# Optimization experiments

Hardware: AMD Instinct MI355X
Metric: run time of the kernel (lower is better)

Reference implementation:

```python
import jax, jax.numpy as jnp
import numpy as np

INPUT_SIZE = 2048
HIDDEN_SIZE = 2048
BATCH = 4096
COMBINED = INPUT_SIZE + HIDDEN_SIZE


def setup_inputs() -> dict:
    key = jax.random.key(0)
    ks = jax.random.split(key, 11)
    s = 1.0 / np.sqrt(COMBINED)  # torch Linear default init scale
    inp = {
        "x_t": jax.random.normal(ks[0], (BATCH, INPUT_SIZE), jnp.float32),
        "h_prev": jax.random.normal(ks[1], (BATCH, HIDDEN_SIZE), jnp.float32),
        "c_prev": jax.random.normal(ks[2], (BATCH, HIDDEN_SIZE), jnp.float32),
        # torch nn.Linear weights: [out, in]
        "W_f": jax.random.uniform(ks[3], (HIDDEN_SIZE, COMBINED), jnp.float32, -s, s),
        "b_f": jax.random.uniform(ks[4], (HIDDEN_SIZE,), jnp.float32, -s, s),
        "W_i": jax.random.uniform(ks[5], (HIDDEN_SIZE, COMBINED), jnp.float32, -s, s),
        "b_i": jax.random.uniform(ks[6], (HIDDEN_SIZE,), jnp.float32, -s, s),
        "W_c": jax.random.uniform(ks[7], (HIDDEN_SIZE, COMBINED), jnp.float32, -s, s),
        "b_c": jax.random.uniform(ks[8], (HIDDEN_SIZE,), jnp.float32, -s, s),
        "W_o": jax.random.uniform(ks[9], (HIDDEN_SIZE, COMBINED), jnp.float32, -s, s),
        "b_o": jax.random.uniform(ks[10], (HIDDEN_SIZE,), jnp.float32, -s, s),
    }
    return inp


def reference(x_t, h_prev, c_prev, W_f, b_f, W_i, b_i, W_c, b_c, W_o, b_o):
    # combined = cat([h_prev, x_t], dim=1)  -> [B, H + I]
    combined = jnp.concatenate([h_prev, x_t], axis=1)
    # Fuse the four gate GEMMs into one [B, C] x [C, 4H] matmul.
    W = jnp.concatenate([W_f, W_i, W_c, W_o], axis=0)  # [4H, C]
    b = jnp.concatenate([b_f, b_i, b_c, b_o], axis=0)  # [4H]
    gates = combined @ W.T + b  # [B, 4H]
    gf, gi, gc, go = jnp.split(gates, 4, axis=1)
    f_t = jax.nn.sigmoid(gf)
    i_t = jax.nn.sigmoid(gi)
    c_tilde = jnp.tanh(gc)
    o_t = jax.nn.sigmoid(go)
    c_t = f_t * c_prev + i_t * c_tilde
    h_t = o_t * jnp.tanh(c_t)
    return (h_t, c_t)
```

## Files before the change

### kernel.cpp

```cpp
#include <hip/hip_runtime.h>
#include <hip/hip_bf16.h>
#include <cstdint>

#define B_DIM 4096
#define H_DIM 2048
#define I_DIM 2048
#define K_DIM 4096
#define N4    8192

typedef unsigned int u32;
typedef unsigned short u16;
typedef __attribute__((ext_vector_type(4))) float floatx4;
typedef __attribute__((ext_vector_type(8))) short bf16x8;
typedef __attribute__((ext_vector_type(8))) float f32x8;
typedef __attribute__((ext_vector_type(8))) __bf16 bfx8;

__device__ static inline void gload16(const void* g, void* l) {
    __builtin_amdgcn_global_load_lds(
        (const __attribute__((address_space(1))) u32*)g,
        (__attribute__((address_space(3))) u32*)l, 16, 0, 0);
}
__device__ static inline float fast_sig(float x) {
    return 1.f / (1.f + __expf(-x));
}
__device__ static inline float fast_tanh(float x) {
    float ax = fabsf(x);
    float t = __expf(-2.f * ax);
    float r = (1.f - t) / (1.f + t);
    return copysignf(r, x);
}

__global__ void convert_all(const float* __restrict__ h_prev, const float* __restrict__ x_t,
                            const float* __restrict__ Wf, const float* __restrict__ Wi,
                            const float* __restrict__ Wc, const float* __restrict__ Wo,
                            u16* __restrict__ comb, u16* __restrict__ wb) {
    const int bid = blockIdx.x;
    const float* src;
    u16* dst;
    if (bid < 8192) {
        int base = (bid * 256 + (int)threadIdx.x) * 8;
        int row = base >> 12, col = base & 4095;
        src = (col < H_DIM) ? h_prev + (size_t)row * H_DIM + col
                            : x_t    + (size_t)row * I_DIM + (col - H_DIM);
        dst = comb + base;
    } else {
        long long base = ((long long)(bid - 8192) * 256 + threadIdx.x) * 8;
        int n = (int)(base >> 12), col = (int)(base & 4095);
        int row128 = n & 127;
        int g = (row128 >> 4) & 3;
        int j = (n >> 7) * 32 + ((row128 >> 6) << 4) + (row128 & 15);
        const float* W = (g == 0) ? Wf : (g == 1) ? Wi : (g == 2) ? Wc : Wo;
        src = W + (size_t)j * K_DIM + col;
        dst = wb + base;
    }
    float4 v0 = *(const float4*)src;
    float4 v1 = *(const float4*)(src + 4);
    f32x8 f = { v0.x, v0.y, v0.z, v0.w, v1.x, v1.y, v1.z, v1.w };
    *(bfx8*)dst = __builtin_convertvector(f, bfx8);
}

__device__ static inline void stage32(const u16* __restrict__ A, const u16* __restrict__ Bm,
                                      u16* dA, u16* dB, int mb, int nbT, int kt, int tid) {
#pragma unroll
    for (int s = 0; s < 2; ++s) {
        int c = tid + s * 512;
        int row = c >> 2;
        int ko = ((c & 3) ^ ((c >> 3) & 3)) * 8;
        gload16(A + (size_t)(mb + row) * K_DIM + kt + ko, (char*)dA + c * 16);
        gload16(Bm + (size_t)(nbT + row) * K_DIM + kt + ko, (char*)dB + c * 16);
    }
}

__global__ __launch_bounds__(512, 2) void gemm_lstm(const u16* __restrict__ A,
                                                    const u16* __restrict__ Bm,
                                                    const float* __restrict__ c_prev,
                                                    const float* __restrict__ bf_,
                                                    const float* __restrict__ bi_,
                                                    const float* __restrict__ bc_,
                                                    const float* __restrict__ bo_,
                                                    float* __restrict__ out) {
    __shared__ __align__(16) u16 lsA[4][256 * 32];
    __shared__ __align__(16) u16 lsB[4][256 * 32];

    const int tid  = threadIdx.x;
    const int lane = tid & 63;
    const int wave = tid >> 6;
    const int wm2  = (wave >> 2) * 128;
    const int wn2  = (wave & 3) * 64;
    const int quad = lane >> 4;
    const int r    = lane & 15;
    const int qsw  = (quad ^ ((r >> 1) & 3)) * 8;
    const int mb   = blockIdx.y * 256;
    const int nbT  = blockIdx.x * 256;

    floatx4 acc[8][4];
#pragma unroll
    for (int i = 0; i < 8; ++i)
#pragma unroll
        for (int g = 0; g < 4; ++g)
            acc[i][g] = (floatx4){0.f, 0.f, 0.f, 0.f};

#pragma unroll
    for (int pt = 0; pt < 3; ++pt)
        stage32(A, Bm, lsA[pt], lsB[pt], mb, nbT, pt * 32, tid);

#pragma unroll 4
    for (int t = 0; t < 128; ++t) {
        if (t < 126) {
            asm volatile("s_waitcnt vmcnt(8)" ::: "memory");
        } else {
            asm volatile("s_waitcnt vmcnt(0)" ::: "memory");
        }
        __builtin_amdgcn_s_barrier();
        __builtin_amdgcn_sched_barrier(0);

        if (t < 125)
            stage32(A, Bm, lsA[(t + 3) & 3], lsB[(t + 3) & 3], mb, nbT, (t + 3) * 32, tid);

        const u16* sA = lsA[t & 3];
        const u16* sB = lsB[t & 3];
        bf16x8 af[8], bb[4];
#pragma unroll
        for (int i = 0; i < 8; ++i)
            af[i] = *(const bf16x8*)&sA[(wm2 + i * 16 + r) * 32 + qsw];
#pragma unroll
        for (int g = 0; g < 4; ++g)
            bb[g] = *(const bf16x8*)&sB[(wn2 + g * 16 + r) * 32 + qsw];

        __builtin_amdgcn_s_setprio(1);
#pragma unroll
        for (int i = 0; i < 8; ++i)
#pragma unroll
            for (int g = 0; g < 4; ++g)
                acc[i][g] = __builtin_amdgcn_mfma_f32_16x16x32_bf16(
                    af[i], bb[g], acc[i][g], 0, 0, 0);
        __builtin_amdgcn_s_setprio(0);
    }

    __builtin_amdgcn_sched_barrier(0);

    const int j = blockIdx.x * 64 + (wave & 3) * 16 + r;
    const float bfv = bf_[j], biv = bi_[j], bcv = bc_[j], bov = bo_[j];
    const int rowb = mb + wm2 + quad * 4;
    const float* cp = c_prev + (size_t)rowb * H_DIM + j;
    float* oh = out + (size_t)rowb * H_DIM + j;
    float* oc = oh + (size_t)B_DIM * H_DIM;
#pragma unroll
    for (int i = 0; i < 8; ++i) {
#pragma unroll
        for (int rg = 0; rg < 4; ++rg) {
            size_t off = (size_t)(i * 16 + rg) * H_DIM;
            float gf = acc[i][0][rg] + bfv;
            float gi = acc[i][1][rg] + biv;
            float gc = acc[i][2][rg] + bcv;
            float go = acc[i][3][rg] + bov;
            float f  = fast_sig(gf);
            float ii = fast_sig(gi);
            float ct = fast_tanh(gc);
            float oo = fast_sig(go);
            float c  = f * cp[off] + ii * ct;
            float h  = oo * fast_tanh(c);
            oh[off] = h;
            oc[off] = c;
        }
    }
}

__global__ void lstm_naive(const float* __restrict__ x_t, const float* __restrict__ h_prev,
                           const float* __restrict__ c_prev,
                           const float* __restrict__ Wf, const float* __restrict__ bf_,
                           const float* __restrict__ Wi, const float* __restrict__ bi_,
                           const float* __restrict__ Wc, const float* __restrict__ bc_,
                           const float* __restrict__ Wo, const float* __restrict__ bo_,
                           float* __restrict__ out) {
    int j = blockIdx.x * blockDim.x + threadIdx.x;
    int b = blockIdx.y;
    const float* hrow = h_prev + (long long)b * H_DIM;
    const float* xrow = x_t   + (long long)b * I_DIM;
    const float* wf = Wf + (long long)j * K_DIM;
    const float* wi = Wi + (long long)j * K_DIM;
    const float* wc = Wc + (long long)j * K_DIM;
    const float* wo = Wo + (long long)j * K_DIM;
    float af = bf_[j], ai = bi_[j], ac = bc_[j], ao = bo_[j];
    for (int k = 0; k < H_DIM; k += 4) {
        float4 v = *(const float4*)(hrow + k);
        float4 a = *(const float4*)(wf + k);
        float4 bqi = *(const float4*)(wi + k);
        float4 cq = *(const float4*)(wc + k);
        float4 dq = *(const float4*)(wo + k);
        af += v.x*a.x + v.y*a.y + v.z*a.z + v.w*a.w;
        ai += v.x*bqi.x + v.y*bqi.y + v.z*bqi.z + v.w*bqi.w;
        ac += v.x*cq.x + v.y*cq.y + v.z*cq.z + v.w*cq.w;
        ao += v.x*dq.x + v.y*dq.y + v.z*dq.z + v.w*dq.w;
    }
    for (int k = 0; k < I_DIM; k += 4) {
        float4 v = *(const float4*)(xrow + k);
        float4 a = *(const float4*)(wf + H_DIM + k);
        float4 bqi = *(const float4*)(wi + H_DIM + k);
        float4 cq = *(const float4*)(wc + H_DIM + k);
        float4 dq = *(const float4*)(wo + H_DIM + k);
        af += v.x*a.x + v.y*a.y + v.z*a.z + v.w*a.w;
        ai += v.x*bqi.x + v.y*bqi.y + v.z*bqi.z + v.w*bqi.w;
        ac += v.x*cq.x + v.y*cq.y + v.z*cq.z + v.w*cq.w;
        ao += v.x*dq.x + v.y*dq.y + v.z*dq.z + v.w*dq.w;
    }
    float f  = 1.f / (1.f + __expf(-af));
    float ii = 1.f / (1.f + __expf(-ai));
    float ct = tanhf(ac);
    float oo = 1.f / (1.f + __expf(-ao));
    int t = b * H_DIM + j;
    float c = f * c_prev[t] + ii * ct;
    out[t] = oo * tanhf(c);
    out[B_DIM * H_DIM + t] = c;
}

extern "C" void kernel_launch(void* const* d_in, const int* in_sizes, int n_in,
                              void* d_out, int out_size, void* d_ws, size_t ws_size,
                              hipStream_t stream) {
    const float* x_t    = (const float*)d_in[0];
    const float* h_prev = (const float*)d_in[1];
    const float* c_prev = (const float*)d_in[2];
    const float* Wf = (const float*)d_in[3];  const float* bf_ = (const float*)d_in[4];
    const float* Wi = (const float*)d_in[5];  const float* bi_ = (const float*)d_in[6];
    const float* Wc = (const float*)d_in[7];  const float* bc_ = (const float*)d_in[8];
    const float* Wo = (const float*)d_in[9];  const float* bo_ = (const float*)d_in[10];
    float* out = (float*)d_out;

    const size_t comb_elems = (size_t)B_DIM * K_DIM;
    const size_t wb_elems   = (size_t)N4 * K_DIM;
    const size_t need = (comb_elems + wb_elems) * sizeof(u16);

    if (ws_size >= need) {
        u16* comb = (u16*)d_ws;
        u16* wb   = comb + comb_elems;
        convert_all<<<24576, 256, 0, stream>>>(h_prev, x_t, Wf, Wi, Wc, Wo, comb, wb);
        dim3 grid(N4 / 256, B_DIM / 256);
        gemm_lstm<<<grid, 512, 0, stream>>>(comb, wb, c_prev, bf_, bi_, bc_, bo_, out);
    } else {
        dim3 grid(H_DIM / 256, B_DIM);
        lstm_naive<<<grid, 256, 0, stream>>>(x_t, h_prev, c_prev,
                                             Wf, bf_, Wi, bi_, Wc, bc_, Wo, bo_, out);
    }
}
```

Before: 489.8 us.

## Double-buffer LDS fragments in GEMM main loop and grid-stride the convert kernel

The GEMM main loop now loads the next K-step's A/B fragments from LDS into a second register set while MFMAs run on the current set, a software-pipelined ping-pong with a peeled prologue and epilogue. Global-load addresses are precomputed per thread, so each stage only adds an offset. The convert kernel becomes a grid-stride loop launched with far fewer blocks. The aim is to hide LDS read latency behind MFMA and cut address and launch overhead, at the cost of more VGPRs, which may hurt occupancy at 2 blocks of 512 threads.

```diff
diff --git a/kernel.cpp b/kernel.cpp
--- a/kernel.cpp
+++ b/kernel.cpp
@@ -30,46 +30,69 @@
     return copysignf(r, x);
 }
 
-__global__ void convert_all(const float* __restrict__ h_prev, const float* __restrict__ x_t,
-                            const float* __restrict__ Wf, const float* __restrict__ Wi,
-                            const float* __restrict__ Wc, const float* __restrict__ Wo,
-                            u16* __restrict__ comb, u16* __restrict__ wb) {
-    const int bid = blockIdx.x;
-    const float* src;
-    u16* dst;
-    if (bid < 8192) {
-        int base = (bid * 256 + (int)threadIdx.x) * 8;
-        int row = base >> 12, col = base & 4095;
-        src = (col < H_DIM) ? h_prev + (size_t)row * H_DIM + col
-                            : x_t    + (size_t)row * I_DIM + (col - H_DIM);
-        dst = comb + base;
-    } else {
-        long long base = ((long long)(bid - 8192) * 256 + threadIdx.x) * 8;
-        int n = (int)(base >> 12), col = (int)(base & 4095);
-        int row128 = n & 127;
-        int g = (row128 >> 4) & 3;
-        int j = (n >> 7) * 32 + ((row128 >> 6) << 4) + (row128 & 15);
-        const float* W = (g == 0) ? Wf : (g == 1) ? Wi : (g == 2) ? Wc : Wo;
-        src = W + (size_t)j * K_DIM + col;
-        dst = wb + base;
-    }
-    float4 v0 = *(const float4*)src;
-    float4 v1 = *(const float4*)(src + 4);
-    f32x8 f = { v0.x, v0.y, v0.z, v0.w, v1.x, v1.y, v1.z, v1.w };
-    *(bfx8*)dst = __builtin_convertvector(f, bfx8);
-}
-
-__device__ static inline void stage32(const u16* __restrict__ A, const u16* __restrict__ Bm,
-                                      u16* dA, u16* dB, int mb, int nbT, int kt, int tid) {
-#pragma unroll
-    for (int s = 0; s < 2; ++s) {
-        int c = tid + s * 512;
-        int row = c >> 2;
-        int ko = ((c & 3) ^ ((c >> 3) & 3)) * 8;
-        gload16(A + (size_t)(mb + row) * K_DIM + kt + ko, (char*)dA + c * 16);
-        gload16(Bm + (size_t)(nbT + row) * K_DIM + kt + ko, (char*)dB + c * 16);
-    }
-}
+__global__ __launch_bounds__(256) void convert_all(
+        const float* __restrict__ h_prev, const float* __restrict__ x_t,
+        const float* __restrict__ Wf, const float* __restrict__ Wi,
+        const float* __restrict__ Wc, const float* __restrict__ Wo,
+        u16* __restrict__ comb, u16* __restrict__ wb) {
+    const long long NCHUNK = ((long long)B_DIM * K_DIM + (long long)N4 * K_DIM) / 8;
+    for (long long ci = (long long)blockIdx.x * 256 + threadIdx.x; ci < NCHUNK;
+         ci += (long long)gridDim.x * 256) {
+        long long e = ci * 8;
+        const float* src;
+        u16* dst;
+        if (e < (long long)B_DIM * K_DIM) {
+            int base = (int)e;
+            int row = base >> 12, col = base & 4095;
+            src = (col < H_DIM) ? h_prev + (size_t)row * H_DIM + col
+                                : x_t    + (size_t)row * I_DIM + (col - H_DIM);
+            dst = comb + base;
+        } else {
+            long long base = e - (long long)B_DIM * K_DIM;
+            int n = (int)(base >> 12), col = (int)(base & 4095);
+            int row128 = n & 127;
+            int g = (row128 >> 4) & 3;
+            int j = (n >> 7) * 32 + ((row128 >> 6) << 4) + (row128 & 15);
+            const float* W = (g == 0) ? Wf : (g == 1) ? Wi : (g == 2) ? Wc : Wo;
+            src = W + (size_t)j * K_DIM + col;
+            dst = wb + base;
+        }
+        float4 v0 = *(const float4*)src;
+        float4 v1 = *(const float4*)(src + 4);
+        f32x8 f = { v0.x, v0.y, v0.z, v0.w, v1.x, v1.y, v1.z, v1.w };
+        *(bfx8*)dst = __builtin_convertvector(f, bfx8);
+    }
+}
+
+__device__ static inline void stage32(const u16* aSrc, const u16* bSrc,
+                                      char* dA, char* dB, int doff) {
+    gload16(aSrc,                dA + doff);
+    gload16(aSrc + 128 * K_DIM,  dA + doff + 8192);
+    gload16(bSrc,                dB + doff);
+    gload16(bSrc + 128 * K_DIM,  dB + doff + 8192);
+}
+
+#define GBODY(T, FCA, FCB, FNA, FNB, VMN, DOSTAGE)                               \
+  {                                                                              \
+    asm volatile("s_waitcnt vmcnt(" #VMN ")" ::: "memory");                      \
+    __builtin_amdgcn_s_barrier();                                                \
+    __builtin_amdgcn_sched_barrier(0);                                           \
+    if (DOSTAGE)                                                                 \
+      stage32(aSrc + ((T) + 3) * 32, bSrc + ((T) + 3) * 32,                      \
+              (char*)lsA[((T) + 3) & 3], (char*)lsB[((T) + 3) & 3], doff);       \
+    const u16* sA_ = lsA[((T) + 1) & 3];                                         \
+    const u16* sB_ = lsB[((T) + 1) & 3];                                         \
+    _Pragma("unroll") for (int i_ = 0; i_ < 8; ++i_)                             \
+      FNA[i_] = *(const bf16x8*)&sA_[(wm2 + i_ * 16 + r) * 32 + qsw];            \
+    _Pragma("unroll") for (int g_ = 0; g_ < 4; ++g_)                             \
+      FNB[g_] = *(const bf16x8*)&sB_[(wn2 + g_ * 16 + r) * 32 + qsw];            \
+    __builtin_amdgcn_s_setprio(1);                                               \
+    _Pragma("unroll") for (int i_ = 0; i_ < 8; ++i_)                             \
+      _Pragma("unroll") for (int g_ = 0; g_ < 4; ++g_)                           \
+        acc[i_][g_] = __builtin_amdgcn_mfma_f32_16x16x32_bf16(                   \
+            FCA[i_], FCB[g_], acc[i_][g_], 0, 0, 0);                             \
+    __builtin_amdgcn_s_setprio(0);                                               \
+  }
 
 __global__ __launch_bounds__(512, 2) void gemm_lstm(const u16* __restrict__ A,
                                                     const u16* __restrict__ Bm,
@@ -93,6 +116,11 @@
     const int mb   = blockIdx.y * 256;
     const int nbT  = blockIdx.x * 256;
 
+    const int ko = ((tid & 3) ^ ((tid >> 3) & 3)) * 8;
+    const u16* aSrc = A  + (size_t)(mb  + (tid >> 2)) * K_DIM + ko;
+    const u16* bSrc = Bm + (size_t)(nbT + (tid >> 2)) * K_DIM + ko;
+    const int doff = tid * 16;
+
     floatx4 acc[8][4];
 #pragma unroll
     for (int i = 0; i < 8; ++i)
@@ -102,40 +130,39 @@
 
 #pragma unroll
     for (int pt = 0; pt < 3; ++pt)
-        stage32(A, Bm, lsA[pt], lsB[pt], mb, nbT, pt * 32, tid);
-
-#pragma unroll 4
-    for (int t = 0; t < 128; ++t) {
-        if (t < 126) {
-            asm volatile("s_waitcnt vmcnt(8)" ::: "memory");
-        } else {
-            asm volatile("s_waitcnt vmcnt(0)" ::: "memory");
-        }
-        __builtin_amdgcn_s_barrier();
-        __builtin_amdgcn_sched_barrier(0);
-
-        if (t < 125)
-            stage32(A, Bm, lsA[(t + 3) & 3], lsB[(t + 3) & 3], mb, nbT, (t + 3) * 32, tid);
-
-        const u16* sA = lsA[t & 3];
-        const u16* sB = lsB[t & 3];
-        bf16x8 af[8], bb[4];
+        stage32(aSrc + pt * 32, bSrc + pt * 32, (char*)lsA[pt], (char*)lsB[pt], doff);
+
+    asm volatile("s_waitcnt vmcnt(8)" ::: "memory");
+    __builtin_amdgcn_s_barrier();
+
+    bf16x8 fA0[8], fB0[4], fA1[8], fB1[4];
+    {
+        const u16* sA = lsA[0];
+        const u16* sB = lsB[0];
 #pragma unroll
         for (int i = 0; i < 8; ++i)
-            af[i] = *(const bf16x8*)&sA[(wm2 + i * 16 + r) * 32 + qsw];
+            fA0[i] = *(const bf16x8*)&sA[(wm2 + i * 16 + r) * 32 + qsw];
 #pragma unroll
         for (int g = 0; g < 4; ++g)
-            bb[g] = *(const bf16x8*)&sB[(wn2 + g * 16 + r) * 32 + qsw];
-
-        __builtin_amdgcn_s_setprio(1);
-#pragma unroll
-        for (int i = 0; i < 8; ++i)
-#pragma unroll
-            for (int g = 0; g < 4; ++g)
-                acc[i][g] = __builtin_amdgcn_mfma_f32_16x16x32_bf16(
-                    af[i], bb[g], acc[i][g], 0, 0, 0);
-        __builtin_amdgcn_s_setprio(0);
-    }
+            fB0[g] = *(const bf16x8*)&sB[(wn2 + g * 16 + r) * 32 + qsw];
+    }
+
+#pragma unroll 1
+    for (int t = 0; t < 124; t += 2) {
+        GBODY(t,     fA0, fB0, fA1, fB1, 4, 1);
+        GBODY(t + 1, fA1, fB1, fA0, fB0, 4, 1);
+    }
+    GBODY(124, fA0, fB0, fA1, fB1, 4, 1);
+    GBODY(125, fA1, fB1, fA0, fB0, 4, 0);
+    GBODY(126, fA0, fB0, fA1, fB1, 0, 0);
+    __builtin_amdgcn_s_setprio(1);
+#pragma unroll
+    for (int i = 0; i < 8; ++i)
+#pragma unroll
+        for (int g = 0; g < 4; ++g)
+            acc[i][g] = __builtin_amdgcn_mfma_f32_16x16x32_bf16(
+                fA1[i], fB1[g], acc[i][g], 0, 0, 0);
+    __builtin_amdgcn_s_setprio(0);
 
     __builtin_amdgcn_sched_barrier(0);
 
@@ -233,7 +260,7 @@
     if (ws_size >= need) {
         u16* comb = (u16*)d_ws;
         u16* wb   = comb + comb_elems;
-        convert_all<<<24576, 256, 0, stream>>>(h_prev, x_t, Wf, Wi, Wc, Wo, comb, wb);
+        convert_all<<<2048, 256, 0, stream>>>(h_prev, x_t, Wf, Wi, Wc, Wo, comb, wb);
         dim3 grid(N4 / 256, B_DIM / 256);
         gemm_lstm<<<grid, 512, 0, stream>>>(comb, wb, c_prev, bf_, bi_, bc_, bo_, out);
     } else {
```

Result: slower. 541.1 us (+10.5%).

## Fuse fp32-to-bf16 conversion into GEMM loads and drop the conversion pass

Applied to the files above, without the earlier changes.

The separate pass that converted activations and weights to bf16 in workspace is removed. The GEMM now streams fp32 tiles directly from h_prev/x_t and the four weight matrices into LDS, and converts to bf16 when building MFMA fragments. It also adds a block-index swizzle for cache locality and switches from a 4-stage to a 2-stage LDS pipeline. This saves the extra global round trip of the conversion kernel. In exchange it doubles the bytes per tile from global memory and LDS (128KB of LDS per block, which limits occupancy) and gives shallower prefetch with a full vmcnt(0) wait each step.

```diff
diff --git a/kernel.cpp b/kernel.cpp
--- a/kernel.cpp
+++ b/kernel.cpp
@@ -29,58 +29,56 @@
     float r = (1.f - t) / (1.f + t);
     return copysignf(r, x);
 }
-
-__global__ void convert_all(const float* __restrict__ h_prev, const float* __restrict__ x_t,
-                            const float* __restrict__ Wf, const float* __restrict__ Wi,
-                            const float* __restrict__ Wc, const float* __restrict__ Wo,
-                            u16* __restrict__ comb, u16* __restrict__ wb) {
-    const int bid = blockIdx.x;
-    const float* src;
-    u16* dst;
-    if (bid < 8192) {
-        int base = (bid * 256 + (int)threadIdx.x) * 8;
-        int row = base >> 12, col = base & 4095;
-        src = (col < H_DIM) ? h_prev + (size_t)row * H_DIM + col
-                            : x_t    + (size_t)row * I_DIM + (col - H_DIM);
-        dst = comb + base;
-    } else {
-        long long base = ((long long)(bid - 8192) * 256 + threadIdx.x) * 8;
-        int n = (int)(base >> 12), col = (int)(base & 4095);
-        int row128 = n & 127;
-        int g = (row128 >> 4) & 3;
-        int j = (n >> 7) * 32 + ((row128 >> 6) << 4) + (row128 & 15);
-        const float* W = (g == 0) ? Wf : (g == 1) ? Wi : (g == 2) ? Wc : Wo;
-        src = W + (size_t)j * K_DIM + col;
-        dst = wb + base;
-    }
-    float4 v0 = *(const float4*)src;
-    float4 v1 = *(const float4*)(src + 4);
-    f32x8 f = { v0.x, v0.y, v0.z, v0.w, v1.x, v1.y, v1.z, v1.w };
-    *(bfx8*)dst = __builtin_convertvector(f, bfx8);
+__device__ static inline bf16x8 pack8(float4 lo, float4 hi) {
+    f32x8 t = { lo.x, lo.y, lo.z, lo.w, hi.x, hi.y, hi.z, hi.w };
+    bfx8 b = __builtin_convertvector(t, bfx8);
+    bf16x8 rr;
+    __builtin_memcpy(&rr, &b, sizeof(rr));
+    return rr;
 }
 
-__device__ static inline void stage32(const u16* __restrict__ A, const u16* __restrict__ Bm,
-                                      u16* dA, u16* dB, int mb, int nbT, int kt, int tid) {
-#pragma unroll
-    for (int s = 0; s < 2; ++s) {
-        int c = tid + s * 512;
-        int row = c >> 2;
-        int ko = ((c & 3) ^ ((c >> 3) & 3)) * 8;
-        gload16(A + (size_t)(mb + row) * K_DIM + kt + ko, (char*)dA + c * 16);
-        gload16(Bm + (size_t)(nbT + row) * K_DIM + kt + ko, (char*)dB + c * 16);
-    }
-}
+#define STAGE(T, NA, NB)                                                        \
+  { _Pragma("unroll") for (int s_ = 0; s_ < 4; ++s_) {                          \
+      const float* sa_ = (((T) < 64) ? h_prev : xmh) + aoff[s_] + (T) * 32;     \
+      gload16(sa_, (char*)(NA) + (tid + s_ * 512) * 16);                        \
+      gload16(bptr[s_] + (T) * 32, (char*)(NB) + (tid + s_ * 512) * 16);        \
+  } }
 
-__global__ __launch_bounds__(512, 2) void gemm_lstm(const u16* __restrict__ A,
-                                                    const u16* __restrict__ Bm,
-                                                    const float* __restrict__ c_prev,
-                                                    const float* __restrict__ bf_,
-                                                    const float* __restrict__ bi_,
-                                                    const float* __restrict__ bc_,
-                                                    const float* __restrict__ bo_,
-                                                    float* __restrict__ out) {
-    __shared__ __align__(16) u16 lsA[4][256 * 32];
-    __shared__ __align__(16) u16 lsB[4][256 * 32];
+#define BODY(T, CA, CB, NA, NB)                                                 \
+  {                                                                             \
+    asm volatile("s_waitcnt vmcnt(0)" ::: "memory");                            \
+    __builtin_amdgcn_s_barrier();                                               \
+    __builtin_amdgcn_sched_barrier(0);                                          \
+    if ((T) + 1 < 128) STAGE((T) + 1, NA, NB);                                  \
+    bf16x8 af_[8], bb_[4];                                                      \
+    _Pragma("unroll") for (int i_ = 0; i_ < 8; ++i_) {                          \
+      const float* pa_ = (CA) + (wm2 + i_ * 16 + r) * 32;                       \
+      af_[i_] = pack8(*(const float4*)(pa_ + s0q), *(const float4*)(pa_ + s1q)); \
+    }                                                                           \
+    _Pragma("unroll") for (int g_ = 0; g_ < 4; ++g_) {                          \
+      const float* pb_ = (CB) + (wn2 + g_ * 16 + r) * 32;                       \
+      bb_[g_] = pack8(*(const float4*)(pb_ + s0q), *(const float4*)(pb_ + s1q)); \
+    }                                                                           \
+    __builtin_amdgcn_s_setprio(1);                                              \
+    _Pragma("unroll") for (int i_ = 0; i_ < 8; ++i_)                            \
+      _Pragma("unroll") for (int g_ = 0; g_ < 4; ++g_)                          \
+        acc[i_][g_] = __builtin_amdgcn_mfma_f32_16x16x32_bf16(                  \
+            af_[i_], bb_[g_], acc[i_][g_], 0, 0, 0);                            \
+    __builtin_amdgcn_s_setprio(0);                                              \
+  }
+
+__global__ __launch_bounds__(512, 2) void gemm_lstm(
+        const float* __restrict__ x_t, const float* __restrict__ h_prev,
+        const float* __restrict__ c_prev,
+        const float* __restrict__ Wf, const float* __restrict__ Wi,
+        const float* __restrict__ Wc, const float* __restrict__ Wo,
+        const float* __restrict__ bf_, const float* __restrict__ bi_,
+        const float* __restrict__ bc_, const float* __restrict__ bo_,
+        float* __restrict__ out) {
+    __shared__ __align__(16) float lsA0[256 * 32];
+    __shared__ __align__(16) float lsB0[256 * 32];
+    __shared__ __align__(16) float lsA1[256 * 32];
+    __shared__ __align__(16) float lsB1[256 * 32];
 
     const int tid  = threadIdx.x;
     const int lane = tid & 63;
@@ -89,9 +87,33 @@
     const int wn2  = (wave & 3) * 64;
     const int quad = lane >> 4;
     const int r    = lane & 15;
-    const int qsw  = (quad ^ ((r >> 1) & 3)) * 8;
-    const int mb   = blockIdx.y * 256;
-    const int nbT  = blockIdx.x * 256;
+    const int rx   = r & 7;
+    const int s0q  = ((2 * quad)     ^ rx) * 4;
+    const int s1q  = ((2 * quad + 1) ^ rx) * 4;
+
+    const int lin = blockIdx.y * gridDim.x + blockIdx.x;
+    const int swz = (lin & 7) * 64 + (lin >> 3);
+    const int bx  = swz & 31;
+    const int by  = swz >> 5;
+    const int mb  = by * 256;
+    const int nbT = bx * 256;
+
+    int aoff[4];
+    const float* bptr[4];
+#pragma unroll
+    for (int s = 0; s < 4; ++s) {
+        int c   = tid + s * 512;
+        int row = c >> 3;
+        int sw  = ((c & 7) ^ (row & 7)) * 4;
+        aoff[s] = (mb + row) * H_DIM + sw;
+        int n      = nbT + row;
+        int row128 = n & 127;
+        int g      = (row128 >> 4) & 3;
+        int j      = (n >> 7) * 32 + ((row128 >> 6) << 4) + (row128 & 15);
+        const float* W = (g == 0) ? Wf : (g == 1) ? Wi : (g == 2) ? Wc : Wo;
+        bptr[s] = W + (size_t)j * K_DIM + sw;
+    }
+    const float* xmh = x_t - H_DIM;
 
     floatx4 acc[8][4];
 #pragma unroll
@@ -100,46 +122,17 @@
         for (int g = 0; g < 4; ++g)
             acc[i][g] = (floatx4){0.f, 0.f, 0.f, 0.f};
 
-#pragma unroll
-    for (int pt = 0; pt < 3; ++pt)
-        stage32(A, Bm, lsA[pt], lsB[pt], mb, nbT, pt * 32, tid);
+    STAGE(0, lsA0, lsB0);
 
-#pragma unroll 4
-    for (int t = 0; t < 128; ++t) {
-        if (t < 126) {
-            asm volatile("s_waitcnt vmcnt(8)" ::: "memory");
-        } else {
-            asm volatile("s_waitcnt vmcnt(0)" ::: "memory");
-        }
-        __builtin_amdgcn_s_barrier();
-        __builtin_amdgcn_sched_barrier(0);
-
-        if (t < 125)
-            stage32(A, Bm, lsA[(t + 3) & 3], lsB[(t + 3) & 3], mb, nbT, (t + 3) * 32, tid);
-
-        const u16* sA = lsA[t & 3];
-        const u16* sB = lsB[t & 3];
-        bf16x8 af[8], bb[4];
-#pragma unroll
-        for (int i = 0; i < 8; ++i)
-            af[i] = *(const bf16x8*)&sA[(wm2 + i * 16 + r) * 32 + qsw];
-#pragma unroll
-        for (int g = 0; g < 4; ++g)
-            bb[g] = *(const bf16x8*)&sB[(wn2 + g * 16 + r) * 32 + qsw];
-
-        __builtin_amdgcn_s_setprio(1);
-#pragma unroll
-        for (int i = 0; i < 8; ++i)
-#pragma unroll
-            for (int g = 0; g < 4; ++g)
-                acc[i][g] = __builtin_amdgcn_mfma_f32_16x16x32_bf16(
-                    af[i], bb[g], acc[i][g], 0, 0, 0);
-        __builtin_amdgcn_s_setprio(0);
+#pragma unroll 1
+    for (int t = 0; t < 128; t += 2) {
+        BODY(t,     lsA0, lsB0, lsA1, lsB1);
+        BODY(t + 1, lsA1, lsB1, lsA0, lsB0);
     }
 
     __builtin_amdgcn_sched_barrier(0);
 
-    const int j = blockIdx.x * 64 + (wave & 3) * 16 + r;
+    const int j = bx * 64 + (wave & 3) * 16 + r;
     const float bfv = bf_[j], biv = bi_[j], bcv = bc_[j], bov = bo_[j];
     const int rowb = mb + wm2 + quad * 4;
     const float* cp = c_prev + (size_t)rowb * H_DIM + j;
@@ -166,54 +159,6 @@
     }
 }
 
-__global__ void lstm_naive(const float* __restrict__ x_t, const float* __restrict__ h_prev,
-                           const float* __restrict__ c_prev,
-                           const float* __restrict__ Wf, const float* __restrict__ bf_,
-                           const float* __restrict__ Wi, const float* __restrict__ bi_,
-                           const float* __restrict__ Wc, const float* __restrict__ bc_,
-                           const float* __restrict__ Wo, const float* __restrict__ bo_,
-                           float* __restrict__ out) {
-    int j = blockIdx.x * blockDim.x + threadIdx.x;
-    int b = blockIdx.y;
-    const float* hrow = h_prev + (long long)b * H_DIM;
-    const float* xrow = x_t   + (long long)b * I_DIM;
-    const float* wf = Wf + (long long)j * K_DIM;
-    const float* wi = Wi + (long long)j * K_DIM;
-    const float* wc = Wc + (long long)j * K_DIM;
-    const float* wo = Wo + (long long)j * K_DIM;
-    float af = bf_[j], ai = bi_[j], ac = bc_[j], ao = bo_[j];
-    for (int k = 0; k < H_DIM; k += 4) {
-        float4 v = *(const float4*)(hrow + k);
-        float4 a = *(const float4*)(wf + k);
-        float4 bqi = *(const float4*)(wi + k);
-        float4 cq = *(const float4*)(wc + k);
-        float4 dq = *(const float4*)(wo + k);
-        af += v.x*a.x + v.y*a.y + v.z*a.z + v.w*a.w;
-        ai += v.x*bqi.x + v.y*bqi.y + v.z*bqi.z + v.w*bqi.w;
-        ac += v.x*cq.x + v.y*cq.y + v.z*cq.z + v.w*cq.w;
-        ao += v.x*dq.x + v.y*dq.y + v.z*dq.z + v.w*dq.w;
-    }
-    for (int k = 0; k < I_DIM; k += 4) {
-        float4 v = *(const float4*)(xrow + k);
-        float4 a = *(const float4*)(wf + H_DIM + k);
-        float4 bqi = *(const float4*)(wi + H_DIM + k);
-        float4 cq = *(const float4*)(wc + H_DIM + k);
-        float4 dq = *(const float4*)(wo + H_DIM + k);
-        af += v.x*a.x + v.y*a.y + v.z*a.z + v.w*a.w;
-        ai += v.x*bqi.x + v.y*bqi.y + v.z*bqi.z + v.w*bqi.w;
-        ac += v.x*cq.x + v.y*cq.y + v.z*cq.z + v.w*cq.w;
-        ao += v.x*dq.x + v.y*dq.y + v.z*dq.z + v.w*dq.w;
-    }
-    float f  = 1.f / (1.f + __expf(-af));
-    float ii = 1.f / (1.f + __expf(-ai));
-    float ct = tanhf(ac);
-    float oo = 1.f / (1.f + __expf(-ao));
-    int t = b * H_DIM + j;
-    float c = f * c_prev[t] + ii * ct;
-    out[t] = oo * tanhf(c);
-    out[B_DIM * H_DIM + t] = c;
-}
-
 extern "C" void kernel_launch(void* const* d_in, const int* in_sizes, int n_in,
                               void* d_out, int out_size, void* d_ws, size_t ws_size,
                               hipStream_t stream) {
@@ -226,19 +171,8 @@
     const float* Wo = (const float*)d_in[9];  const float* bo_ = (const float*)d_in[10];
     float* out = (float*)d_out;
 
-    const size_t comb_elems = (size_t)B_DIM * K_DIM;
-    const size_t wb_elems   = (size_t)N4 * K_DIM;
-    const size_t need = (comb_elems + wb_elems) * sizeof(u16);
-
-    if (ws_size >= need) {
-        u16* comb = (u16*)d_ws;
-        u16* wb   = comb + comb_elems;
-        convert_all<<<24576, 256, 0, stream>>>(h_prev, x_t, Wf, Wi, Wc, Wo, comb, wb);
-        dim3 grid(N4 / 256, B_DIM / 256);
-        gemm_lstm<<<grid, 512, 0, stream>>>(comb, wb, c_prev, bf_, bi_, bc_, bo_, out);
-    } else {
-        dim3 grid(H_DIM / 256, B_DIM);
-        lstm_naive<<<grid, 256, 0, stream>>>(x_t, h_prev, c_prev,
-                                             Wf, bf_, Wi, bi_, Wc, bc_, Wo, bo_, out);
-    }
+    dim3 grid(N4 / 256, B_DIM / 256);
+    gemm_lstm<<<grid, 512, 0, stream>>>(x_t, h_prev, c_prev,
+                                        Wf, Wi, Wc, Wo,
+                                        bf_, bi_, bc_, bo_, out);
 }
```

New measurement: 713.3 us. +45.6%, slower.

## Split each K-tile into two MFMA halves interleaved with staggered global-to-LDS loads

Applied to the files above, without the earlier changes.

The 32-wide K-step body is rewritten as a macro that issues the A-tile global-to-LDS loads first and runs MFMAs on the upper 4 row-fragments. It then loads the lower A fragments, issues the B-tile loads, passes a second barrier and runs the remaining 16 MFMAs. Per-thread source and LDS addresses are precomputed once, and the final iterations are peeled so the staging branch is removed from the loop. The aim is to spread memory issue across MFMA work and reduce peak fragment register use. In exchange it adds a second workgroup barrier per tile and drops loop unrolling, which may add sync overhead.

```diff
diff --git a/kernel.cpp b/kernel.cpp
--- a/kernel.cpp
+++ b/kernel.cpp
@@ -59,17 +59,47 @@
     *(bfx8*)dst = __builtin_convertvector(f, bfx8);
 }
 
-__device__ static inline void stage32(const u16* __restrict__ A, const u16* __restrict__ Bm,
-                                      u16* dA, u16* dB, int mb, int nbT, int kt, int tid) {
-#pragma unroll
-    for (int s = 0; s < 2; ++s) {
-        int c = tid + s * 512;
-        int row = c >> 2;
-        int ko = ((c & 3) ^ ((c >> 3) & 3)) * 8;
-        gload16(A + (size_t)(mb + row) * K_DIM + kt + ko, (char*)dA + c * 16);
-        gload16(Bm + (size_t)(nbT + row) * K_DIM + kt + ko, (char*)dB + c * 16);
-    }
-}
+#define TILE(T, VMS, DOSTAGE)                                                   \
+  {                                                                             \
+    asm volatile("s_waitcnt vmcnt(" VMS ")" ::: "memory");                      \
+    __builtin_amdgcn_s_barrier();                                               \
+    __builtin_amdgcn_sched_barrier(0);                                          \
+    const u16* sA_ = lsA[(T) & 3];                                              \
+    const u16* sB_ = lsB[(T) & 3];                                              \
+    if (DOSTAGE) {                                                              \
+      const u16* as_ = aSrc + ((T) + 3) * 32;                                   \
+      char* dA_ = (char*)lsA[((T) + 3) & 3] + doff;                             \
+      gload16(as_, dA_);                                                        \
+      gload16(as_ + 128 * K_DIM, dA_ + 8192);                                   \
+    }                                                                           \
+    bf16x8 afL_[4], afH_[4], bb_[4];                                            \
+    _Pragma("unroll") for (int i_ = 0; i_ < 4; ++i_)                            \
+      afL_[i_] = *(const bf16x8*)&sA_[(wm2 + i_ * 16 + r) * 32 + qsw];          \
+    _Pragma("unroll") for (int g_ = 0; g_ < 4; ++g_)                            \
+      bb_[g_] = *(const bf16x8*)&sB_[(wn2 + g_ * 16 + r) * 32 + qsw];           \
+    __builtin_amdgcn_s_setprio(1);                                              \
+    _Pragma("unroll") for (int i_ = 0; i_ < 4; ++i_)                            \
+      _Pragma("unroll") for (int g_ = 0; g_ < 4; ++g_)                          \
+        acc[i_][g_] = __builtin_amdgcn_mfma_f32_16x16x32_bf16(                  \
+            afL_[i_], bb_[g_], acc[i_][g_], 0, 0, 0);                           \
+    __builtin_amdgcn_s_setprio(0);                                              \
+    _Pragma("unroll") for (int i_ = 0; i_ < 4; ++i_)                            \
+      afH_[i_] = *(const bf16x8*)&sA_[(wm2 + 64 + i_ * 16 + r) * 32 + qsw];     \
+    if (DOSTAGE) {                                                              \
+      const u16* bs_ = bSrc + ((T) + 3) * 32;                                   \
+      char* dB_ = (char*)lsB[((T) + 3) & 3] + doff;                             \
+      gload16(bs_, dB_);                                                        \
+      gload16(bs_ + 128 * K_DIM, dB_ + 8192);                                   \
+    }                                                                           \
+    __builtin_amdgcn_s_barrier();                                               \
+    __builtin_amdgcn_sched_barrier(0);                                          \
+    __builtin_amdgcn_s_setprio(1);                                              \
+    _Pragma("unroll") for (int i_ = 0; i_ < 4; ++i_)                            \
+      _Pragma("unroll") for (int g_ = 0; g_ < 4; ++g_)                          \
+        acc[4 + i_][g_] = __builtin_amdgcn_mfma_f32_16x16x32_bf16(              \
+            afH_[i_], bb_[g_], acc[4 + i_][g_], 0, 0, 0);                       \
+    __builtin_amdgcn_s_setprio(0);                                              \
+  }
 
 __global__ __launch_bounds__(512, 2) void gemm_lstm(const u16* __restrict__ A,
                                                     const u16* __restrict__ Bm,
@@ -93,6 +123,11 @@
     const int mb   = blockIdx.y * 256;
     const int nbT  = blockIdx.x * 256;
 
+    const int ko = ((tid & 3) ^ ((tid >> 3) & 3)) * 8;
+    const u16* aSrc = A  + (size_t)(mb  + (tid >> 2)) * K_DIM + ko;
+    const u16* bSrc = Bm + (size_t)(nbT + (tid >> 2)) * K_DIM + ko;
+    const int doff = tid * 16;
+
     floatx4 acc[8][4];
 #pragma unroll
     for (int i = 0; i < 8; ++i)
@@ -101,41 +136,22 @@
             acc[i][g] = (floatx4){0.f, 0.f, 0.f, 0.f};
 
 #pragma unroll
-    for (int pt = 0; pt < 3; ++pt)
-        stage32(A, Bm, lsA[pt], lsB[pt], mb, nbT, pt * 32, tid);
-
-#pragma unroll 4
-    for (int t = 0; t < 128; ++t) {
-        if (t < 126) {
-            asm volatile("s_waitcnt vmcnt(8)" ::: "memory");
-        } else {
-            asm volatile("s_waitcnt vmcnt(0)" ::: "memory");
-        }
-        __builtin_amdgcn_s_barrier();
-        __builtin_amdgcn_sched_barrier(0);
-
-        if (t < 125)
-            stage32(A, Bm, lsA[(t + 3) & 3], lsB[(t + 3) & 3], mb, nbT, (t + 3) * 32, tid);
-
-        const u16* sA = lsA[t & 3];
-        const u16* sB = lsB[t & 3];
-        bf16x8 af[8], bb[4];
-#pragma unroll
-        for (int i = 0; i < 8; ++i)
-            af[i] = *(const bf16x8*)&sA[(wm2 + i * 16 + r) * 32 + qsw];
-#pragma unroll
-        for (int g = 0; g < 4; ++g)
-            bb[g] = *(const bf16x8*)&sB[(wn2 + g * 16 + r) * 32 + qsw];
-
-        __builtin_amdgcn_s_setprio(1);
-#pragma unroll
-        for (int i = 0; i < 8; ++i)
-#pragma unroll
-            for (int g = 0; g < 4; ++g)
-                acc[i][g] = __builtin_amdgcn_mfma_f32_16x16x32_bf16(
-                    af[i], bb[g], acc[i][g], 0, 0, 0);
-        __builtin_amdgcn_s_setprio(0);
-    }
+    for (int pt = 0; pt < 3; ++pt) {
+        const u16* as_ = aSrc + pt * 32;
+        char* dA_ = (char*)lsA[pt] + doff;
+        gload16(as_, dA_);
+        gload16(as_ + 128 * K_DIM, dA_ + 8192);
+        const u16* bs_ = bSrc + pt * 32;
+        char* dB_ = (char*)lsB[pt] + doff;
+        gload16(bs_, dB_);
+        gload16(bs_ + 128 * K_DIM, dB_ + 8192);
+    }
+
+#pragma unroll 1
+    for (int t = 0; t < 125; ++t) TILE(t, "8", 1);
+    TILE(125, "8", 0);
+    TILE(126, "0", 0);
+    TILE(127, "0", 0);
 
     __builtin_amdgcn_sched_barrier(0);
 
```

Measured after the change: 547.4 us. 1.12x slower.
